# Performance work log

Measured on AMD Instinct MI355X. Metric: run time of the kernel, lower is better.

## Reference

```python
import jax, jax.numpy as jnp
import numpy as np

EPS = 1e-5
H, DA, DM = 8, 64, 128  # num_read_heads, d_address, d_memory

def setup_inputs() -> dict:
    key = jax.random.key(0)
    ks = jax.random.split(key, 10)
    B, T, D, M = 4, 512, 1024, 128
    scale = lambda fan_in: 1.0 / np.sqrt(fan_in)
    return {
        "query": jax.random.normal(ks[0], (B, T, D), jnp.float32),
        "matrix": jax.random.normal(ks[1], (B, M, DA, DM), jnp.float32),
        "normalizer": jax.random.uniform(ks[2], (B, M, DA), jnp.float32),
        "addresses": jax.random.normal(ks[3], (M, DA), jnp.float32),
        "W_access": jax.random.normal(ks[4], (D, H * DA), jnp.float32) * scale(D),
        "b_access": jnp.zeros((H * DA,), jnp.float32),
        "W_read": jax.random.normal(ks[5], (D, H * DA), jnp.float32) * scale(D),
        "b_read": jnp.zeros((H * DA,), jnp.float32),
        "W_merge": jax.random.normal(ks[6], (H * DM, D), jnp.float32) * scale(H * DM),
        "b_merge": jnp.zeros((D,), jnp.float32),
    }

def reference(query, matrix, normalizer, addresses,
              W_access, b_access, W_read, b_read, W_merge, b_merge):
    act = jax.nn.softplus  # linear kernel feature map
    B, T, D = query.shape
    M = matrix.shape[1]

    # head projections -> (B,T,H,DA)
    aq = act((query @ W_access + b_access).reshape(B, T, H, DA))
    rq = act((query @ W_read + b_read).reshape(B, T, H, DA))

    # --- stage 1: linear attention over the num_memories axis ---
    ak = act(addresses)                       # (M,DA) activated keys
    norm_k = jnp.sum(ak, axis=0)              # (DA,) kernel normalizer (shared)
    den1 = jnp.einsum('btha,a->bth', aq, norm_k)[..., None] + EPS  # (B,T,H,1)

    # kernel over flattened matrix values (M, DA*DM)
    kern_m = jnp.einsum('ma,bmx->bax', ak, matrix.reshape(B, M, DA * DM))
    mat2 = jnp.einsum('btha,bax->bthx', aq, kern_m) / den1          # (B,T,H,DA*DM)
    mat2 = mat2.reshape(B, T, H, DA, DM)

    # kernel over normalizer values (M, DA)
    kern_n = jnp.einsum('ma,bmd->bad', ak, normalizer)              # (B,DA,DA)
    norm2 = jnp.einsum('btha,bad->bthd', aq, kern_n) / den1         # (B,T,H,DA)

    # --- stage 2: read from reduced kernel with read query ---
    num = jnp.einsum('btha,bthax->bthx', rq, mat2)                  # (B,T,H,DM)
    den = jnp.einsum('btha,btha->bth', rq, norm2)[..., None] + EPS
    resp = num / den                                                # (B,T,H,DM)

    return resp.reshape(B, T, H * DM) @ W_merge + b_merge           # (B,T,D)
```

## Files before the change

kernel.cpp:

```cpp
#include <hip/hip_runtime.h>
#include <hip/hip_bf16.h>
#include <math.h>

#define EPSF 1e-5f

typedef __attribute__((ext_vector_type(8))) short short8;
typedef __attribute__((ext_vector_type(4))) float f32x4;
typedef _Float16 half8 __attribute__((ext_vector_type(8)));

constexpr int Bc = 4, Tc = 512, Dc = 1024, Mc = 128, Hc = 8, DAc = 64, DMc = 128;
constexpr int BT = Bc * Tc;
constexpr int Xc = DAc * DMc;
constexpr int Rb = Tc * Hc;

__device__ __forceinline__ float softplus_f(float x) {
    return fmaxf(x, 0.f) + log1pf(expf(-fabsf(x)));
}
__device__ __forceinline__ short f2bf(float f) {
    __hip_bfloat16 h = __float2bfloat16(f);
    return *reinterpret_cast<short*>(&h);
}
__device__ __forceinline__ unsigned pk2(float a, float b) {
    return (unsigned)(unsigned short)f2bf(a) | ((unsigned)(unsigned short)f2bf(b) << 16);
}
__device__ __forceinline__ void lds_load16(void* lds, const void* g) {
    __builtin_amdgcn_global_load_lds((const __attribute__((address_space(1))) int*)g,
                                     (__attribute__((address_space(3))) int*)lds, 16, 0, 0);
}

__global__ __launch_bounds__(256) void front_kern(
        const float* __restrict__ addresses,
        const float* __restrict__ matrix,
        const float* __restrict__ normalizer,
        const float* __restrict__ query,
        const float* __restrict__ W_access,
        const float* __restrict__ W_read,
        const float* __restrict__ W_merge,
        _Float16* __restrict__ kern2,
        float* __restrict__ kern_n,
        float* __restrict__ norm_k,
        __hip_bfloat16* __restrict__ qb,
        __hip_bfloat16* __restrict__ WpT,
        __hip_bfloat16* __restrict__ WmT) {
    __shared__ float smem[8192];
    int bid = blockIdx.x;
    int tid = threadIdx.x;

    if (bid < 256) {
        float (*T)[132] = (float(*)[132])smem;
        _Float16 (*At)[40] = (_Float16(*)[40])(smem + 4224);
        int lane = tid & 63, wid = tid >> 6;
        int l15 = lane & 15, lg = lane >> 4;
        int b = bid >> 6, a = bid & 63;
        int wr = wid & 1, wc = wid >> 1;

        half8 bfrag[2][4];
#pragma unroll
        for (int cf = 0; cf < 2; cf++) {
            int a2 = wc * 32 + cf * 16 + l15;
#pragma unroll
            for (int ks = 0; ks < 4; ks++)
#pragma unroll
                for (int j = 0; j < 8; j++) {
                    int mm = ks * 32 + lg * 8 + j;
                    bfrag[cf][ks][j] = (_Float16)softplus_f(addresses[mm * 64 + a2]);
                }
        }

        const float* msrc = matrix + (size_t)b * Mc * Xc + a * DMc;
        int r = tid >> 3, ms = (tid & 7) * 16;
        int tm = tid >> 1, tk0 = (tid & 1) * 16;

        f32x4 acc[4][2];
#pragma unroll
        for (int i = 0; i < 4; i++)
#pragma unroll
            for (int j = 0; j < 2; j++) acc[i][j] = (f32x4){0.f, 0.f, 0.f, 0.f};

        float4 ld[4];
#pragma unroll
        for (int j = 0; j < 4; j++)
            ld[j] = *(const float4*)(msrc + (size_t)r * Xc + ms + j * 4);

        for (int s = 0; s < 4; s++) {
#pragma unroll
            for (int j = 0; j < 4; j++) *(float4*)&T[r][ms + j * 4] = ld[j];
            __syncthreads();
            if (s < 3) {
#pragma unroll
                for (int j = 0; j < 4; j++)
                    ld[j] = *(const float4*)(msrc + (size_t)((s + 1) * 32 + r) * Xc + ms + j * 4);
            }
            {
                half8 lo, hi;
#pragma unroll
                for (int j = 0; j < 8; j++) lo[j] = (_Float16)T[tk0 + j][tm];
#pragma unroll
                for (int j = 0; j < 8; j++) hi[j] = (_Float16)T[tk0 + 8 + j][tm];
                *(half8*)&At[tm][tk0] = lo;
                *(half8*)&At[tm][tk0 + 8] = hi;
            }
            __syncthreads();
#pragma unroll
            for (int rf = 0; rf < 4; rf++) {
                int row = wr * 64 + rf * 16 + l15;
                half8 af = *(const half8*)&At[row][lg * 8];
#pragma unroll
                for (int cf = 0; cf < 2; cf++)
                    acc[rf][cf] = __builtin_amdgcn_mfma_f32_16x16x32_f16(
                        af, bfrag[cf][s], acc[rf][cf], 0, 0, 0);
            }
            __syncthreads();
        }
        _Float16* dst = kern2 + ((size_t)(b * 64 + a)) * Mc * DAc;
#pragma unroll
        for (int rf = 0; rf < 4; rf++)
#pragma unroll
            for (int cf = 0; cf < 2; cf++) {
                int a2 = wc * 32 + cf * 16 + l15;
#pragma unroll
                for (int i = 0; i < 4; i++) {
                    int mrow = wr * 64 + rf * 16 + lg * 4 + i;
                    dst[mrow * DAc + a2] = (_Float16)acc[rf][cf][i];
                }
            }
        return;
    }
    if (bid < 288) {
        int idx = bid - 256;
        int b = idx >> 3, ch = idx & 7;
        for (int i = tid; i < Mc * DAc; i += 256) smem[i] = softplus_f(addresses[i]);
        __syncthreads();
        int d = tid & 63;
        int g = tid >> 6;
        int a2b = ch * 8 + g * 2;
        float acc0 = 0.f, acc1 = 0.f;
        const float* np = normalizer + (size_t)b * Mc * DAc + d;
        for (int mm = 0; mm < Mc; mm++) {
            float v = np[(size_t)mm * DAc];
            acc0 = fmaf(smem[mm * DAc + a2b + 0], v, acc0);
            acc1 = fmaf(smem[mm * DAc + a2b + 1], v, acc1);
        }
        kern_n[((size_t)b * DAc + a2b + 0) * DAc + d] = acc0;
        kern_n[((size_t)b * DAc + a2b + 1) * DAc + d] = acc1;
        return;
    }
    if (bid == 288) {
        for (int i = tid; i < Mc * DAc; i += 256) smem[i] = softplus_f(addresses[i]);
        __syncthreads();
        if (tid < DAc) {
            float s = 0.f;
            for (int mm = 0; mm < Mc; mm++) s += smem[mm * DAc + tid];
            norm_k[tid] = s;
        }
        return;
    }
    if (bid < 2337) {
        int i = ((bid - 289) * 256 + tid) * 4;
        float4 v = *(const float4*)(query + i);
        unsigned* d = (unsigned*)(qb + i);
        d[0] = pk2(v.x, v.y);
        d[1] = pk2(v.z, v.w);
        return;
    }
    float (*tile)[65] = (float(*)[65])smem;
    const float* S; int stride, nb, n0, kt;
    __hip_bfloat16* dst;
    if (bid < 2593) {
        int idx = bid - 2337;
        kt = idx & 15;
        n0 = (idx >> 4) * 64;
        if (n0 < 512) { S = W_access; nb = n0; }
        else          { S = W_read;   nb = n0 - 512; }
        stride = 512;
        dst = WpT;
    } else {
        int idx = bid - 2593;
        kt = idx & 15;
        n0 = (idx >> 4) * 64;
        S = W_merge; nb = n0; stride = 1024;
        dst = WmT;
    }
    {
        int kl = tid >> 2, q = tid & 3;
        const float* src = S + (size_t)(kt * 64 + kl) * stride + nb + q * 16;
#pragma unroll
        for (int j = 0; j < 4; j++) {
            float4 v = *(const float4*)(src + j * 4);
            tile[kl][q * 16 + j * 4 + 0] = v.x;
            tile[kl][q * 16 + j * 4 + 1] = v.y;
            tile[kl][q * 16 + j * 4 + 2] = v.z;
            tile[kl][q * 16 + j * 4 + 3] = v.w;
        }
    }
    __syncthreads();
    {
        int nl = tid >> 2, q = tid & 3;
        unsigned* d = (unsigned*)(dst + (size_t)(n0 + nl) * 1024 + kt * 64 + q * 16);
#pragma unroll
        for (int j = 0; j < 8; j++)
            d[j] = pk2(tile[q * 16 + j * 2][nl], tile[q * 16 + j * 2 + 1][nl]);
    }
}

template <bool SOFTPLUS, typename OutT>
__global__ __launch_bounds__(256) void gemm_bf16(const __hip_bfloat16* __restrict__ A,
                                                 const __hip_bfloat16* __restrict__ BT_,
                                                 const float* __restrict__ bias0,
                                                 const float* __restrict__ bias1, int N0,
                                                 OutT* __restrict__ C, int N, int K) {
    __shared__ short Ab[2][2][64 * 64];
    __shared__ short Bb[2][2][64 * 64];
    int tid = threadIdx.x, lane = tid & 63, wid = tid >> 6;
    int l15 = lane & 15, lg = lane >> 4;
    int rowblk = blockIdx.x * 64, colblk = blockIdx.y * 64;
    int wr = wid & 1, wc = wid >> 1;
    int srow = lane >> 3;
    int sk = ((lane & 7) ^ srow) * 8;

    f32x4 acc[2][2];
#pragma unroll
    for (int i = 0; i < 2; i++)
#pragma unroll
        for (int j = 0; j < 2; j++) acc[i][j] = (f32x4){0.f, 0.f, 0.f, 0.f};

    auto stage = [&](int kbase, int buf, int sub) {
#pragma unroll
        for (int j = 0; j < 2; j++) {
            int c = wid * 2 + j;
            int row = c * 8 + srow;
            lds_load16(&Ab[buf][sub][c * 512], A + (size_t)(rowblk + row) * K + kbase + sk);
            lds_load16(&Bb[buf][sub][c * 512], BT_ + (size_t)(colblk + row) * K + kbase + sk);
        }
    };
    stage(0, 0, 0);
    stage(64, 0, 1);
    __syncthreads();
    int cur = 0;
    int nks = K >> 7;
    for (int ks = 0; ks < nks; ks++) {
        if (ks + 1 < nks) {
            stage((ks + 1) << 7, cur ^ 1, 0);
            stage(((ks + 1) << 7) + 64, cur ^ 1, 1);
        }
#pragma unroll
        for (int sub = 0; sub < 2; sub++) {
#pragma unroll
            for (int kh = 0; kh < 2; kh++) {
                short8 af[2], bfr[2];
#pragma unroll
                for (int rf = 0; rf < 2; rf++) {
                    int row = wr * 32 + rf * 16 + l15;
                    int ksw = (kh * 32 + lg * 8) ^ ((row & 7) << 3);
                    af[rf] = *(const short8*)&Ab[cur][sub][row * 64 + ksw];
                }
#pragma unroll
                for (int cf = 0; cf < 2; cf++) {
                    int col = wc * 32 + cf * 16 + l15;
                    int ksw = (kh * 32 + lg * 8) ^ ((col & 7) << 3);
                    bfr[cf] = *(const short8*)&Bb[cur][sub][col * 64 + ksw];
                }
#pragma unroll
                for (int rf = 0; rf < 2; rf++)
#pragma unroll
                    for (int cf = 0; cf < 2; cf++)
                        acc[rf][cf] = __builtin_amdgcn_mfma_f32_16x16x32_bf16(
                            af[rf], bfr[cf], acc[rf][cf], 0, 0, 0);
            }
        }
        __syncthreads();
        cur ^= 1;
    }
#pragma unroll
    for (int cf = 0; cf < 2; cf++) {
        int col = colblk + wc * 32 + cf * 16 + l15;
        float bv = (col < N0) ? bias0[col] : bias1[col - N0];
#pragma unroll
        for (int rf = 0; rf < 2; rf++) {
            int rbase = rowblk + wr * 32 + rf * 16 + lg * 4;
#pragma unroll
            for (int i = 0; i < 4; i++) {
                float v = acc[rf][cf][i] + bv;
                if (SOFTPLUS) v = softplus_f(v);
                C[(size_t)(rbase + i) * N + col] = (OutT)v;
            }
        }
    }
}

__global__ __launch_bounds__(256) void k4_mfma(const _Float16* __restrict__ aqrq16,
                                               const _Float16* __restrict__ kern2,
                                               const float* __restrict__ kern_n,
                                               const float* __restrict__ norm_k,
                                               __hip_bfloat16* __restrict__ resp) {
    __shared__ _Float16 Bb[2][4][64 * 64];
    __shared__ _Float16 rql[64][72];
    __shared__ float scl[64];
    __shared__ float nkl[64];
    int tid = threadIdx.x, lane = tid & 63, wid = tid >> 6;
    int l15 = lane & 15, lg = lane >> 4;
    int b = blockIdx.x >> 7;
    int rc = (blockIdx.x >> 1) & 63;
    int mh = blockIdx.x & 1;
    int rowbase = rc * 64;
    int wr = wid & 1, wc = wid >> 1;
    float* knl = (float*)&Bb[1][0][0];

    auto stageB = [&](int a_, int buf, int sl) {
#pragma unroll
        for (int j = 0; j < 2; j++) {
            int c = wid * 2 + j;
            int m = c * 8 + (lane >> 3);
            int sa = ((lane & 7) ^ (lane >> 3)) * 8;
            lds_load16(&Bb[buf][sl][c * 512],
                       kern2 + (((size_t)(b * 64 + a_)) * Mc + mh * 64 + m) * DAc + sa);
        }
    };
#pragma unroll
    for (int sl = 0; sl < 4; sl++) stageB(sl, 0, sl);
    {
#pragma unroll
        for (int j = 0; j < 4; j++) {
            int c = wid * 4 + j;
            lds_load16(knl + c * 256, kern_n + (size_t)b * 4096 + c * 256 + lane * 4);
        }
    }

    half8 aqp[2][2];
#pragma unroll
    for (int rf = 0; rf < 2; rf++)
#pragma unroll
        for (int kh = 0; kh < 2; kh++) {
            int rg = rowbase + wr * 32 + rf * 16 + l15;
            int t_ = rg >> 3, h = rg & 7;
            aqp[rf][kh] = *(const half8*)(aqrq16 + ((size_t)(b * Tc + t_)) * 1024
                                          + h * 64 + kh * 32 + lg * 8);
        }
    {
        int row = tid >> 2, q = tid & 3;
        int rg = rowbase + row;
        int t_ = rg >> 3, h = rg & 7;
        const _Float16* src = aqrq16 + ((size_t)(b * Tc + t_)) * 1024 + 512 + h * 64 + q * 16;
        *(half8*)&rql[row][q * 16] = *(const half8*)(src);
        *(half8*)&rql[row][q * 16 + 8] = *(const half8*)(src + 8);
    }
    if (tid < 64) nkl[tid] = norm_k[tid];
    __syncthreads();

    {
        int row = tid >> 2, c = tid & 3;
        int rg = rowbase + row;
        int t_ = rg >> 3, h = rg & 7;
        const _Float16* aqg = aqrq16 + ((size_t)(b * Tc + t_)) * 1024 + h * 64 + c * 16;
        half8 a0 = *(const half8*)(aqg);
        half8 a1 = *(const half8*)(aqg + 8);
        float aqv[16];
#pragma unroll
        for (int j = 0; j < 8; j++) { aqv[j] = (float)a0[j]; aqv[8 + j] = (float)a1[j]; }
        float rqv[64];
#pragma unroll
        for (int j8 = 0; j8 < 8; j8++) {
            half8 v = *(const half8*)&rql[row][j8 * 8];
#pragma unroll
            for (int k = 0; k < 8; k++) rqv[j8 * 8 + k] = (float)v[k];
        }
        float sn = 0.f, d1 = 0.f;
        for (int a2l = 0; a2l < 16; a2l++) {
            int a2 = c * 16 + a2l;
            const float4* kr = (const float4*)(knl + a2 * 64);
            float dot = 0.f;
#pragma unroll
            for (int d4 = 0; d4 < 16; d4++) {
                float4 kv = kr[d4];
                dot = fmaf(kv.x, rqv[d4 * 4 + 0], dot);
                dot = fmaf(kv.y, rqv[d4 * 4 + 1], dot);
                dot = fmaf(kv.z, rqv[d4 * 4 + 2], dot);
                dot = fmaf(kv.w, rqv[d4 * 4 + 3], dot);
            }
            sn = fmaf(aqv[a2l], dot, sn);
            d1 = fmaf(aqv[a2l], nkl[a2], d1);
        }
        sn += __shfl_xor(sn, 1); sn += __shfl_xor(sn, 2);
        d1 += __shfl_xor(d1, 1); d1 += __shfl_xor(d1, 2);
        if (c == 0) {
            float den1 = d1 + EPSF;
            float den = sn / den1 + EPSF;
            scl[row] = 1.f / (den1 * den);
        }
    }
    __syncthreads();

    f32x4 acc[2][2];
#pragma unroll
    for (int i = 0; i < 2; i++)
#pragma unroll
        for (int j = 0; j < 2; j++) acc[i][j] = (f32x4){0.f, 0.f, 0.f, 0.f};

    int cur = 0;
    for (int it = 0; it < 16; it++) {
        if (it < 15) {
#pragma unroll
            for (int sl = 0; sl < 4; sl++) stageB(it * 4 + 4 + sl, cur ^ 1, sl);
        }
#pragma unroll
        for (int as = 0; as < 4; as++) {
            int a = it * 4 + as;
            _Float16 h0 = rql[wr * 32 + l15][a];
            _Float16 h1 = rql[wr * 32 + 16 + l15][a];
            half8 rb0 = {h0, h0, h0, h0, h0, h0, h0, h0};
            half8 rb1 = {h1, h1, h1, h1, h1, h1, h1, h1};
#pragma unroll
            for (int kh = 0; kh < 2; kh++) {
#pragma unroll
                for (int cf = 0; cf < 2; cf++) {
                    int mloc = wc * 32 + cf * 16 + l15;
                    int ch = (kh * 4 + lg) ^ (mloc & 7);
                    half8 bf = *(const half8*)&Bb[cur][as][mloc * 64 + ch * 8];
                    acc[0][cf] = __builtin_amdgcn_mfma_f32_16x16x32_f16(
                        aqp[0][kh] * rb0, bf, acc[0][cf], 0, 0, 0);
                    acc[1][cf] = __builtin_amdgcn_mfma_f32_16x16x32_f16(
                        aqp[1][kh] * rb1, bf, acc[1][cf], 0, 0, 0);
                }
            }
        }
        __syncthreads();
        cur ^= 1;
    }
#pragma unroll
    for (int rf = 0; rf < 2; rf++) {
#pragma unroll
        for (int i = 0; i < 4; i++) {
            int rl = wr * 32 + rf * 16 + lg * 4 + i;
            int rg = rowbase + rl;
            float s = scl[rl];
            int t_ = rg >> 3, h = rg & 7;
            __hip_bfloat16* dst = resp + ((size_t)(b * Tc + t_)) * 1024 + h * DMc + mh * 64;
#pragma unroll
            for (int cf = 0; cf < 2; cf++) {
                int m = wc * 32 + cf * 16 + l15;
                dst[m] = __float2bfloat16(acc[rf][cf][i] * s);
            }
        }
    }
}

extern "C" void kernel_launch(void* const* d_in, const int* in_sizes, int n_in,
                              void* d_out, int out_size, void* d_ws, size_t ws_size,
                              hipStream_t stream) {
    const float* query      = (const float*)d_in[0];
    const float* matrix     = (const float*)d_in[1];
    const float* normalizer = (const float*)d_in[2];
    const float* addresses  = (const float*)d_in[3];
    const float* W_access   = (const float*)d_in[4];
    const float* b_access   = (const float*)d_in[5];
    const float* W_read     = (const float*)d_in[6];
    const float* b_read     = (const float*)d_in[7];
    const float* W_merge    = (const float*)d_in[8];
    const float* b_merge    = (const float*)d_in[9];
    float* out = (float*)d_out;
    (void)in_sizes; (void)n_in; (void)out_size; (void)ws_size;

    float* ws     = (float*)d_ws;
    float* norm_k = ws;
    float* kern_n = ws + 128;
    _Float16* aqrq16 = (_Float16*)(ws + 16512);
    _Float16* kern2  = (_Float16*)(ws + 1065088);
    __hip_bfloat16* qb   = (__hip_bfloat16*)(ws + 2113664);
    __hip_bfloat16* resp = (__hip_bfloat16*)(ws + 3162240);
    __hip_bfloat16* WpT  = (__hip_bfloat16*)(ws + 4210816);
    __hip_bfloat16* WmT  = (__hip_bfloat16*)(ws + 4735104);

    hipLaunchKernelGGL(front_kern, dim3(2849), dim3(256), 0, stream,
                       addresses, matrix, normalizer, query,
                       W_access, W_read, W_merge,
                       kern2, kern_n, norm_k, qb, WpT, WmT);
    hipLaunchKernelGGL((gemm_bf16<true, _Float16>), dim3(32, 16), dim3(256), 0, stream,
                       qb, WpT, b_access, b_read, 512, aqrq16, 1024, 1024);
    hipLaunchKernelGGL(k4_mfma, dim3(512), dim3(256), 0, stream,
                       aqrq16, kern2, kern_n, norm_k, resp);
    hipLaunchKernelGGL((gemm_bf16<false, float>), dim3(32, 16), dim3(256), 0, stream,
                       resp, WmT, b_merge, b_merge, 2048, out, 1024, 1024);
}
```

Measured before the change: 96.51 us.

## Double k4 row tile to 128 rows per block and restructure denominator compute

The k4_mfma kernel now processes 128 rows per block instead of 64, so each staged B tile from kern2 feeds twice as many MFMAs. To fit LDS, the B double-buffer stages 2 address slices per iteration instead of 4, doubling the iteration count. The denominator computation is restructured to accumulate aq·kern_n per column chunk and then dot with rq. Grid size halves to 256 blocks, which reduces parallelism on a large-CU GPU and increases register pressure in exchange for less kern2 reload traffic.

```diff
diff --git a/kernel.cpp b/kernel.cpp
--- a/kernel.cpp
+++ b/kernel.cpp
@@ -293,16 +293,16 @@
                                                const float* __restrict__ kern_n,
                                                const float* __restrict__ norm_k,
                                                __hip_bfloat16* __restrict__ resp) {
-    __shared__ _Float16 Bb[2][4][64 * 64];
-    __shared__ _Float16 rql[64][72];
-    __shared__ float scl[64];
+    __shared__ _Float16 Bb[2][2][64 * 64];
+    __shared__ _Float16 rql[128][72];
+    __shared__ float scl[128];
     __shared__ float nkl[64];
     int tid = threadIdx.x, lane = tid & 63, wid = tid >> 6;
     int l15 = lane & 15, lg = lane >> 4;
-    int b = blockIdx.x >> 7;
-    int rc = (blockIdx.x >> 1) & 63;
+    int b = blockIdx.x >> 6;
+    int rc = (blockIdx.x >> 1) & 31;
     int mh = blockIdx.x & 1;
-    int rowbase = rc * 64;
+    int rowbase = rc * 128;
     int wr = wid & 1, wc = wid >> 1;
     float* knl = (float*)&Bb[1][0][0];
 
@@ -316,8 +316,8 @@
                        kern2 + (((size_t)(b * 64 + a_)) * Mc + mh * 64 + m) * DAc + sa);
         }
     };
-#pragma unroll
-    for (int sl = 0; sl < 4; sl++) stageB(sl, 0, sl);
+    stageB(0, 0, 0);
+    stageB(1, 0, 1);
     {
 #pragma unroll
         for (int j = 0; j < 4; j++) {
@@ -326,62 +326,68 @@
         }
     }
 
-    half8 aqp[2][2];
-#pragma unroll
-    for (int rf = 0; rf < 2; rf++)
+    half8 aqp[4][2];
+#pragma unroll
+    for (int rf = 0; rf < 4; rf++)
 #pragma unroll
         for (int kh = 0; kh < 2; kh++) {
-            int rg = rowbase + wr * 32 + rf * 16 + l15;
+            int rg = rowbase + wr * 64 + rf * 16 + l15;
             int t_ = rg >> 3, h = rg & 7;
             aqp[rf][kh] = *(const half8*)(aqrq16 + ((size_t)(b * Tc + t_)) * 1024
                                           + h * 64 + kh * 32 + lg * 8);
         }
     {
-        int row = tid >> 2, q = tid & 3;
+        int row = tid >> 1, q = tid & 1;
         int rg = rowbase + row;
         int t_ = rg >> 3, h = rg & 7;
-        const _Float16* src = aqrq16 + ((size_t)(b * Tc + t_)) * 1024 + 512 + h * 64 + q * 16;
-        *(half8*)&rql[row][q * 16] = *(const half8*)(src);
-        *(half8*)&rql[row][q * 16 + 8] = *(const half8*)(src + 8);
+        const _Float16* src = aqrq16 + ((size_t)(b * Tc + t_)) * 1024 + 512 + h * 64 + q * 32;
+#pragma unroll
+        for (int k = 0; k < 4; k++)
+            *(half8*)&rql[row][q * 32 + k * 8] = *(const half8*)(src + k * 8);
     }
     if (tid < 64) nkl[tid] = norm_k[tid];
     __syncthreads();
 
-    {
-        int row = tid >> 2, c = tid & 3;
+#pragma unroll
+    for (int half = 0; half < 2; half++) {
+        int row = half * 64 + wid * 16 + (lane >> 2);
+        int c = lane & 3;
         int rg = rowbase + row;
         int t_ = rg >> 3, h = rg & 7;
-        const _Float16* aqg = aqrq16 + ((size_t)(b * Tc + t_)) * 1024 + h * 64 + c * 16;
-        half8 a0 = *(const half8*)(aqg);
-        half8 a1 = *(const half8*)(aqg + 8);
-        float aqv[16];
-#pragma unroll
-        for (int j = 0; j < 8; j++) { aqv[j] = (float)a0[j]; aqv[8 + j] = (float)a1[j]; }
-        float rqv[64];
-#pragma unroll
-        for (int j8 = 0; j8 < 8; j8++) {
-            half8 v = *(const half8*)&rql[row][j8 * 8];
-#pragma unroll
-            for (int k = 0; k < 8; k++) rqv[j8 * 8 + k] = (float)v[k];
-        }
-        float sn = 0.f, d1 = 0.f;
-        for (int a2l = 0; a2l < 16; a2l++) {
-            int a2 = c * 16 + a2l;
-            const float4* kr = (const float4*)(knl + a2 * 64);
-            float dot = 0.f;
-#pragma unroll
-            for (int d4 = 0; d4 < 16; d4++) {
-                float4 kv = kr[d4];
-                dot = fmaf(kv.x, rqv[d4 * 4 + 0], dot);
-                dot = fmaf(kv.y, rqv[d4 * 4 + 1], dot);
-                dot = fmaf(kv.z, rqv[d4 * 4 + 2], dot);
-                dot = fmaf(kv.w, rqv[d4 * 4 + 3], dot);
-            }
-            sn = fmaf(aqv[a2l], dot, sn);
-            d1 = fmaf(aqv[a2l], nkl[a2], d1);
-        }
-        sn += __shfl_xor(sn, 1); sn += __shfl_xor(sn, 2);
-        d1 += __shfl_xor(d1, 1); d1 += __shfl_xor(d1, 2);
+        const _Float16* aqg = aqrq16 + ((size_t)(b * Tc + t_)) * 1024 + h * 64;
+        float accj[16];
+#pragma unroll
+        for (int j = 0; j < 16; j++) accj[j] = 0.f;
+        float d1 = 0.f;
+#pragma unroll
+        for (int a2c = 0; a2c < 4; a2c++) {
+            half8 aa0 = *(const half8*)(aqg + a2c * 16);
+            half8 aa1 = *(const half8*)(aqg + a2c * 16 + 8);
+            float aqv[16];
+#pragma unroll
+            for (int j = 0; j < 8; j++) { aqv[j] = (float)aa0[j]; aqv[8 + j] = (float)aa1[j]; }
+#pragma unroll
+            for (int a2l = 0; a2l < 16; a2l++) {
+                int a2 = a2c * 16 + a2l;
+                float av = aqv[a2l];
+                d1 = fmaf(av, nkl[a2], d1);
+                const float4* kr = (const float4*)(knl + a2 * 64 + c * 16);
+#pragma unroll
+                for (int j4 = 0; j4 < 4; j4++) {
+                    float4 kv = kr[j4];
+                    accj[j4 * 4 + 0] = fmaf(av, kv.x, accj[j4 * 4 + 0]);
+                    accj[j4 * 4 + 1] = fmaf(av, kv.y, accj[j4 * 4 + 1]);
+                    accj[j4 * 4 + 2] = fmaf(av, kv.z, accj[j4 * 4 + 2]);
+                    accj[j4 * 4 + 3] = fmaf(av, kv.w, accj[j4 * 4 + 3]);
+                }
+            }
+        }
+        float sn = 0.f;
+#pragma unroll
+        for (int j = 0; j < 16; j++)
+            sn = fmaf((float)rql[row][c * 16 + j], accj[j], sn);
+        sn += __shfl_xor(sn, 1);
+        sn += __shfl_xor(sn, 2);
         if (c == 0) {
             float den1 = d1 + EPSF;
             float den = sn / den1 + EPSF;
@@ -390,25 +396,27 @@
     }
     __syncthreads();
 
-    f32x4 acc[2][2];
-#pragma unroll
-    for (int i = 0; i < 2; i++)
+    f32x4 acc[4][2];
+#pragma unroll
+    for (int i = 0; i < 4; i++)
 #pragma unroll
         for (int j = 0; j < 2; j++) acc[i][j] = (f32x4){0.f, 0.f, 0.f, 0.f};
 
     int cur = 0;
-    for (int it = 0; it < 16; it++) {
-        if (it < 15) {
-#pragma unroll
-            for (int sl = 0; sl < 4; sl++) stageB(it * 4 + 4 + sl, cur ^ 1, sl);
-        }
-#pragma unroll
-        for (int as = 0; as < 4; as++) {
-            int a = it * 4 + as;
-            _Float16 h0 = rql[wr * 32 + l15][a];
-            _Float16 h1 = rql[wr * 32 + 16 + l15][a];
-            half8 rb0 = {h0, h0, h0, h0, h0, h0, h0, h0};
-            half8 rb1 = {h1, h1, h1, h1, h1, h1, h1, h1};
+    for (int it = 0; it < 32; it++) {
+        if (it < 31) {
+            stageB(it * 2 + 2, cur ^ 1, 0);
+            stageB(it * 2 + 3, cur ^ 1, 1);
+        }
+#pragma unroll
+        for (int as = 0; as < 2; as++) {
+            int a = it * 2 + as;
+            half8 rb[4];
+#pragma unroll
+            for (int rf = 0; rf < 4; rf++) {
+                _Float16 hv = rql[wr * 64 + rf * 16 + l15][a];
+                rb[rf] = (half8){hv, hv, hv, hv, hv, hv, hv, hv};
+            }
 #pragma unroll
             for (int kh = 0; kh < 2; kh++) {
 #pragma unroll
@@ -416,10 +424,10 @@
                     int mloc = wc * 32 + cf * 16 + l15;
                     int ch = (kh * 4 + lg) ^ (mloc & 7);
                     half8 bf = *(const half8*)&Bb[cur][as][mloc * 64 + ch * 8];
-                    acc[0][cf] = __builtin_amdgcn_mfma_f32_16x16x32_f16(
-                        aqp[0][kh] * rb0, bf, acc[0][cf], 0, 0, 0);
-                    acc[1][cf] = __builtin_amdgcn_mfma_f32_16x16x32_f16(
-                        aqp[1][kh] * rb1, bf, acc[1][cf], 0, 0, 0);
+#pragma unroll
+                    for (int rf = 0; rf < 4; rf++)
+                        acc[rf][cf] = __builtin_amdgcn_mfma_f32_16x16x32_f16(
+                            aqp[rf][kh] * rb[rf], bf, acc[rf][cf], 0, 0, 0);
                 }
             }
         }
@@ -427,10 +435,10 @@
         cur ^= 1;
     }
 #pragma unroll
-    for (int rf = 0; rf < 2; rf++) {
+    for (int rf = 0; rf < 4; rf++) {
 #pragma unroll
         for (int i = 0; i < 4; i++) {
-            int rl = wr * 32 + rf * 16 + lg * 4 + i;
+            int rl = wr * 64 + rf * 16 + lg * 4 + i;
             int rg = rowbase + rl;
             float s = scl[rl];
             int t_ = rg >> 3, h = rg & 7;
@@ -476,7 +484,7 @@
                        kern2, kern_n, norm_k, qb, WpT, WmT);
     hipLaunchKernelGGL((gemm_bf16<true, _Float16>), dim3(32, 16), dim3(256), 0, stream,
                        qb, WpT, b_access, b_read, 512, aqrq16, 1024, 1024);
-    hipLaunchKernelGGL(k4_mfma, dim3(512), dim3(256), 0, stream,
+    hipLaunchKernelGGL(k4_mfma, dim3(256), dim3(256), 0, stream,
                        aqrq16, kern2, kern_n, norm_k, resp);
     hipLaunchKernelGGL((gemm_bf16<false, float>), dim3(32, 16), dim3(256), 0, stream,
                        resp, WmT, b_merge, b_merge, 2048, out, 1024, 1024);
```

Result: slower. 100.9 us (+4.6%).
